# Kernel optimization log

Measured on AMD Instinct MI355X. Metric: run time of the kernel, lower is better.

The kernel has to match this reference:

```python
import jax, jax.numpy as jnp
import numpy as np

HEADS = 4


def setup_inputs() -> dict:
    key = jax.random.key(0)
    kx, kqkv, kbq, ko, kbo = jax.random.split(key, 5)
    B, C, H, W = 4, 256, 64, 64
    x = jax.random.normal(kx, (B, C, H, W), dtype=jnp.float32)
    # torch nn.Linear stores weight as [out_features, in_features]
    w_qkv = jax.random.normal(kqkv, (3 * C, C), dtype=jnp.float32) * (1.0 / np.sqrt(C))
    b_qkv = jax.random.normal(kbq, (3 * C,), dtype=jnp.float32) * 0.02
    w_o = jax.random.normal(ko, (C, C), dtype=jnp.float32) * (1.0 / np.sqrt(C))
    b_o = jax.random.normal(kbo, (C,), dtype=jnp.float32) * 0.02
    return {"x": x, "w_qkv": w_qkv, "b_qkv": b_qkv, "w_o": w_o, "b_o": b_o}


def reference(x, w_qkv, b_qkv, w_o, b_o):
    B, C, H, W = x.shape
    S = H * W
    hd = C // HEADS
    # (B, C, H, W) -> (B, S, C)
    xt = x.reshape(B, C, S).transpose(0, 2, 1)
    qkv = xt @ w_qkv.T + b_qkv                      # (B, S, 3C)
    q, k, v = jnp.split(qkv, 3, axis=-1)
    def to_heads(t):
        return t.reshape(B, S, HEADS, hd).transpose(0, 2, 1, 3)  # (B, h, S, hd)
    q, k, v = to_heads(q), to_heads(k), to_heads(v)
    scores = jnp.einsum('bhqd,bhkd->bhqk', q, k) / jnp.sqrt(jnp.float32(hd))
    attn = jax.nn.softmax(scores, axis=-1)          # dropout inactive (eval)
    out = jnp.einsum('bhqk,bhkd->bhqd', attn, v)    # (B, h, S, hd)
    out = out.transpose(0, 2, 1, 3).reshape(B, S, C)
    y = out @ w_o.T + b_o                            # (B, S, C)
    y = y.reshape(B, H, W, C).transpose(0, 3, 1, 2)  # (B, C, H, W)
    return y
```

## Files before the change

### kernel.cpp

```cpp
#include <hip/hip_runtime.h>
#include <stdint.h>

#define DI __device__ __forceinline__

typedef __attribute__((ext_vector_type(8))) __bf16 bf16x8;
typedef __attribute__((ext_vector_type(8))) unsigned short u16x8;
typedef __attribute__((ext_vector_type(4))) float f32x4;
typedef __attribute__((ext_vector_type(4))) uint32_t u32x4;
typedef unsigned short u16;

constexpr int Bb = 4, Cc = 256, Ss = 4096, HD = 64;
constexpr int ELEMS = Bb * Cc * Ss;

DI float bf2f(u16 h) { union { unsigned u; float f; } x; x.u = ((unsigned)h) << 16; return x.f; }
DI u16 f2bf(float f) {
  union { float f; unsigned u; } x; x.f = f;
  return (u16)((x.u + 0x7FFFu + ((x.u >> 16) & 1u)) >> 16);
}
DI uint32_t pack2bf_trunc(float a, float b) {
  union { float f; uint32_t u; } xa, xb;
  xa.f = a; xb.f = b;
  return __builtin_amdgcn_perm(xb.u, xa.u, 0x07060302u);
}
DI bf16x8 ldfrag(const u16* p) { return __builtin_bit_cast(bf16x8, *(const u16x8*)p); }

__global__ __launch_bounds__(256) void k_transpose(const float* __restrict__ x, u16* __restrict__ xt,
                                                   const float* __restrict__ wq, const float* __restrict__ wo,
                                                   u16* __restrict__ wqb, u16* __restrict__ wob) {
  __shared__ u16 T[64][72];
  const int st = blockIdx.x, ct = blockIdx.y, b = blockIdx.z;
  const int tid = threadIdx.x;
  {
    int flat = blockIdx.x + 64 * blockIdx.y + 256 * blockIdx.z;
    int widx = flat * 256 + tid;
    if (widx < 196608) wqb[widx] = f2bf(wq[widx]);
    else wob[widx - 196608] = f2bf(wo[widx - 196608]);
  }
#pragma unroll
  for (int e = 0; e < 2; e++) {
    int ss = tid + e * 256;
    int r = ss >> 3, seg = ss & 7;
    size_t base = ((size_t)(b * Cc + ct * 64 + r) << 12) + st * 64 + seg * 8;
    u16x8 t;
#pragma unroll
    for (int j = 0; j < 8; j++) t[j] = f2bf(x[base + j]);
    *(u16x8*)&T[r][(seg ^ ((r >> 3) & 7)) * 8] = t;
  }
  __syncthreads();
#pragma unroll
  for (int e = 0; e < 2; e++) {
    int ss = tid + e * 256;
    int sr = ss >> 3, cseg = ss & 7;
    u16x8 o;
#pragma unroll
    for (int j = 0; j < 8; j++) {
      int row = cseg * 8 + j;
      o[j] = T[row][(((sr >> 3) ^ cseg) * 8) + (sr & 7)];
    }
    *(u16x8*)(xt + ((size_t)(b * Ss + st * 64 + sr) << 8) + ct * 64 + cseg * 8) = o;
  }
}

DI void stage_tile(const u16* __restrict__ src, int pitch, int r0, int k0, u16 (*dst)[40], int tid) {
#pragma unroll
  for (int e = 0; e < 2; e++) {
    int c = tid + e * 256;
    int row = c >> 2, seg = c & 3;
    u16x8 t = *(const u16x8*)(src + (size_t)(r0 + row) * pitch + k0 + seg * 8);
    *(u16x8*)&dst[row][seg * 8] = t;
  }
}

__global__ __launch_bounds__(256) void k_qkv(const u16* __restrict__ xt, const u16* __restrict__ w,
                                             const float* __restrict__ bias,
                                             u16* __restrict__ q, u16* __restrict__ kk_, u16* __restrict__ vv_) {
  __shared__ u16 As[128][40], Bs[128][40];
  const int tid = threadIdx.x;
  const int wv = tid >> 6, lane = tid & 63;
  const int wm = wv >> 1, wn = wv & 1;
  const int lr = lane & 15, quad = lane >> 4;
  const int r0 = blockIdx.x * 128;
  const int j0 = blockIdx.y * 128;
  f32x4 acc[4][4] = {};
  for (int k0 = 0; k0 < 256; k0 += 32) {
    __syncthreads();
    stage_tile(xt, 256, r0, k0, As, tid);
    stage_tile(w, 256, j0, k0, Bs, tid);
    __syncthreads();
    bf16x8 a[4], b[4];
#pragma unroll
    for (int mt = 0; mt < 4; mt++) a[mt] = ldfrag(&As[wm * 64 + mt * 16 + lr][quad * 8]);
#pragma unroll
    for (int nt = 0; nt < 4; nt++) b[nt] = ldfrag(&Bs[wn * 64 + nt * 16 + lr][quad * 8]);
#pragma unroll
    for (int mt = 0; mt < 4; mt++)
#pragma unroll
      for (int nt = 0; nt < 4; nt++)
        acc[mt][nt] = __builtin_amdgcn_mfma_f32_16x16x32_bf16(a[mt], b[nt], acc[mt][nt], 0, 0, 0);
  }
#pragma unroll
  for (int nt = 0; nt < 4; nt++) {
    int j = j0 + wn * 64 + nt * 16 + lr;
    float bj = bias[j];
    int part = j >> 8, cc = j & 255, head = cc >> 6, d = cc & 63;
    u16* outp = (part == 0) ? q : (part == 1) ? kk_ : vv_;
    float sc = (part == 0) ? 0.18033688f : 1.0f;
#pragma unroll
    for (int mt = 0; mt < 4; mt++)
#pragma unroll
      for (int rg = 0; rg < 4; rg++) {
        int row = r0 + wm * 64 + mt * 16 + quad * 4 + rg;
        int b_ = row >> 12, s = row & 4095;
        outp[((size_t)((b_ * 4 + head) * Ss + s) << 6) + d] = f2bf((acc[mt][nt][rg] + bj) * sc);
      }
  }
}

__global__ __launch_bounds__(256) void k_vt(const u16* __restrict__ v, u16* __restrict__ vt) {
  __shared__ u16 T[64][72];
  const int chunk = blockIdx.x, bh = blockIdx.y;
  const int tid = threadIdx.x;
#pragma unroll
  for (int e = 0; e < 2; e++) {
    int row = (tid >> 3) + e * 32, seg = tid & 7;
    *(u16x8*)&T[row][(seg ^ ((row >> 3) & 7)) * 8] =
        *(const u16x8*)(v + ((size_t)(bh * Ss + chunk * 64 + row) << 6) + seg * 8);
  }
  __syncthreads();
#pragma unroll
  for (int e = 0; e < 2; e++) {
    int d = (tid >> 3) + e * 32, seg = tid & 7;
    u16x8 o;
#pragma unroll
    for (int j = 0; j < 8; j++) {
      int slot = seg * 8 + j;
      int t = (((slot >> 5) & 1) << 1) | ((slot >> 2) & 1);
      int w6 = t * 16 + (((slot >> 3) & 3) << 2) + (slot & 3);
      o[j] = T[w6][(((d >> 3) ^ ((w6 >> 3) & 7)) * 8) + (d & 7)];
    }
    *(u16x8*)(vt + ((size_t)(bh * 64 + d) << 12) + chunk * 64 + seg * 8) = o;
  }
}

__global__ __launch_bounds__(256, 2) void k_attn(const u16* __restrict__ Q, const u16* __restrict__ K,
                                                 const u16* __restrict__ VT, u16* __restrict__ AO,
                                                 u16* __restrict__ AOP, float* __restrict__ lpart,
                                                 int nsplit) {
  __shared__ u16 Kl[2][64][72];
  __shared__ u16 Vl[2][64][72];
  const int tid = threadIdx.x;
  const int wv = tid >> 6, lane = tid & 63;
  const int lr = lane & 15, quad = lane >> 4;
  const int bh = blockIdx.y;
  const int b_ = bh >> 2, head = bh & 3;
  const int qbase = blockIdx.x * 256 + wv * 64;
  const int sp = blockIdx.z;
  const int nchunk = 64 / nsplit, kcg0 = sp * nchunk;
  const u16* Qh = Q + (size_t)bh * Ss * HD;
  const u16* Kh = K + (size_t)bh * Ss * HD;
  const u16* Vh = VT + (size_t)bh * HD * Ss;

  bf16x8 qb[4][2];
#pragma unroll
  for (int nt = 0; nt < 4; nt++)
#pragma unroll
    for (int ks = 0; ks < 2; ks++)
      qb[nt][ks] = ldfrag(Qh + (size_t)(qbase + nt * 16 + lr) * HD + ks * 32 + quad * 8);

  u16x8 ov;
#pragma unroll
  for (int j = 0; j < 8; j++) ov[j] = 0x3F80;
  const bf16x8 ones = __builtin_bit_cast(bf16x8, ov);

  f32x4 O[4][4] = {};
  f32x4 lacc[4] = {};

  u16x8 pf[4];
  const int srow = tid >> 3, sseg = tid & 7;
  auto load_chunk = [&](int kc) {
#pragma unroll
    for (int e = 0; e < 2; e++) {
      pf[e] = *(const u16x8*)(Kh + ((size_t)((kcg0 + kc) * 64 + srow + e * 32) << 6) + sseg * 8);
      pf[2 + e] = *(const u16x8*)(Vh + ((size_t)(srow + e * 32) << 12) + (kcg0 + kc) * 64 + sseg * 8);
    }
  };
  auto store_chunk = [&](int buf) {
#pragma unroll
    for (int e = 0; e < 2; e++) {
      *(u16x8*)&Kl[buf][srow + e * 32][sseg * 8] = pf[e];
      *(u16x8*)&Vl[buf][srow + e * 32][sseg * 8] = pf[2 + e];
    }
  };

  load_chunk(0);
  store_chunk(0);
  if (nchunk > 1) load_chunk(1);
  __syncthreads();

  for (int kc = 0; kc < nchunk; kc++) {
    const int cur = kc & 1;
    if (kc + 1 < nchunk) {
      store_chunk(cur ^ 1);
      if (kc + 2 < nchunk) load_chunk(kc + 2);
    }

    f32x4 St[4][4] = {};
#pragma unroll
    for (int ks = 0; ks < 2; ks++) {
      bf16x8 ka[4];
#pragma unroll
      for (int kt = 0; kt < 4; kt++) ka[kt] = ldfrag(&Kl[cur][kt * 16 + lr][ks * 32 + quad * 8]);
#pragma unroll
      for (int kt = 0; kt < 4; kt++)
#pragma unroll
        for (int nt = 0; nt < 4; nt++)
          St[kt][nt] = __builtin_amdgcn_mfma_f32_16x16x32_bf16(ka[kt], qb[nt][ks], St[kt][nt], 0, 0, 0);
    }

    uint32_t pk[4][4][2];
#pragma unroll
    for (int kt = 0; kt < 4; kt++)
#pragma unroll
      for (int nt = 0; nt < 4; nt++) {
        float p0 = __builtin_amdgcn_exp2f(St[kt][nt][0]);
        float p1 = __builtin_amdgcn_exp2f(St[kt][nt][1]);
        float p2 = __builtin_amdgcn_exp2f(St[kt][nt][2]);
        float p3 = __builtin_amdgcn_exp2f(St[kt][nt][3]);
        pk[kt][nt][0] = pack2bf_trunc(p0, p1);
        pk[kt][nt][1] = pack2bf_trunc(p2, p3);
      }

#pragma unroll
    for (int ks = 0; ks < 2; ks++) {
      bf16x8 pa[4];
#pragma unroll
      for (int mt = 0; mt < 4; mt++) {
        u32x4 t = {pk[2 * ks][mt][0], pk[2 * ks][mt][1], pk[2 * ks + 1][mt][0], pk[2 * ks + 1][mt][1]};
        pa[mt] = __builtin_bit_cast(bf16x8, t);
      }
#pragma unroll
      for (int dt = 0; dt < 4; dt++) {
        bf16x8 vb = ldfrag(&Vl[cur][dt * 16 + lr][ks * 32 + quad * 8]);
#pragma unroll
        for (int mt = 0; mt < 4; mt++)
          O[mt][dt] = __builtin_amdgcn_mfma_f32_16x16x32_bf16(pa[mt], vb, O[mt][dt], 0, 0, 0);
      }
#pragma unroll
      for (int mt = 0; mt < 4; mt++)
        lacc[mt] = __builtin_amdgcn_mfma_f32_16x16x32_bf16(pa[mt], ones, lacc[mt], 0, 0, 0);
    }

    __syncthreads();
  }

  u16* dst = (nsplit == 1) ? AO : (AOP + (size_t)sp * ELEMS);
  if (nsplit > 1 && lr == 0) {
    float* lp = lpart + (size_t)sp * (16 * Ss) + bh * Ss;
#pragma unroll
    for (int mt = 0; mt < 4; mt++)
#pragma unroll
      for (int rg = 0; rg < 4; rg++) lp[qbase + mt * 16 + quad * 4 + rg] = lacc[mt][rg];
  }
#pragma unroll
  for (int mt = 0; mt < 4; mt++)
#pragma unroll
    for (int rg = 0; rg < 4; rg++) {
      float inv = 1.0f / lacc[mt][rg];
      int s = qbase + mt * 16 + quad * 4 + rg;
#pragma unroll
      for (int dt = 0; dt < 4; dt++)
        dst[((size_t)(b_ * Ss + s) << 8) + head * 64 + dt * 16 + lr] = f2bf(O[mt][dt][rg] * inv);
    }
}

__global__ __launch_bounds__(512) void k_oproj(const u16* __restrict__ wo, const u16* __restrict__ ao,
                                               const u16* __restrict__ AOP, const float* __restrict__ lpart,
                                               const float* __restrict__ bo, float* __restrict__ y, int nsplit) {
  __shared__ u16 As[256][40], Bs[128][40];
  const int tid = threadIdx.x;
  const int wv = tid >> 6, lane = tid & 63;
  const int wm = wv >> 1, wn = wv & 1;
  const int lr = lane & 15, quad = lane >> 4;
  const int n0 = blockIdx.x * 128;
  f32x4 acc[4][4] = {};
  for (int k0 = 0; k0 < 256; k0 += 32) {
    __syncthreads();
#pragma unroll
    for (int e = 0; e < 2; e++) {
      int c = tid + e * 512;
      int row = c >> 2, seg = c & 3;
      *(u16x8*)&As[row][seg * 8] = *(const u16x8*)(wo + row * 256 + k0 + seg * 8);
    }
    {
      int row = tid >> 2, seg = tid & 3;
      int bs = n0 + row, cc = k0 + seg * 8;
      u16x8 t;
      if (nsplit == 1) {
        t = *(const u16x8*)(ao + ((size_t)bs << 8) + cc);
      } else {
        int b = bs >> 12, s = bs & 4095, head = cc >> 6;
        int li = (b * 4 + head) * Ss + s;
        u16x8 a0 = *(const u16x8*)(AOP + ((size_t)bs << 8) + cc);
        u16x8 a1 = *(const u16x8*)(AOP + (size_t)ELEMS + ((size_t)bs << 8) + cc);
        float l0 = lpart[li], l1 = lpart[16 * Ss + li];
        float inv = 1.0f / (l0 + l1);
        float w0 = l0 * inv, w1 = l1 * inv;
#pragma unroll
        for (int i = 0; i < 8; i++) t[i] = f2bf(w0 * bf2f(a0[i]) + w1 * bf2f(a1[i]));
      }
      *(u16x8*)&Bs[row][seg * 8] = t;
    }
    __syncthreads();
    bf16x8 a[4], b[4];
#pragma unroll
    for (int mt = 0; mt < 4; mt++) a[mt] = ldfrag(&As[wm * 64 + mt * 16 + lr][quad * 8]);
#pragma unroll
    for (int nt = 0; nt < 4; nt++) b[nt] = ldfrag(&Bs[wn * 64 + nt * 16 + lr][quad * 8]);
#pragma unroll
    for (int mt = 0; mt < 4; mt++)
#pragma unroll
      for (int nt = 0; nt < 4; nt++)
        acc[mt][nt] = __builtin_amdgcn_mfma_f32_16x16x32_bf16(a[mt], b[nt], acc[mt][nt], 0, 0, 0);
  }
#pragma unroll
  for (int mt = 0; mt < 4; mt++)
#pragma unroll
    for (int rg = 0; rg < 4; rg++) {
      int c = wm * 64 + mt * 16 + quad * 4 + rg;
      float bc = bo[c];
#pragma unroll
      for (int nt = 0; nt < 4; nt++) {
        int col = n0 + wn * 64 + nt * 16 + lr;
        int b_ = col >> 12, s = col & 4095;
        y[((size_t)(b_ * Cc + c) << 12) + s] = acc[mt][nt][rg] + bc;
      }
    }
}

extern "C" void kernel_launch(void* const* d_in, const int* in_sizes, int n_in,
                              void* d_out, int out_size, void* d_ws, size_t ws_size,
                              hipStream_t stream) {
  const float* x = (const float*)d_in[0];
  const float* w_qkv = (const float*)d_in[1];
  const float* b_qkv = (const float*)d_in[2];
  const float* w_o = (const float*)d_in[3];
  const float* b_o = (const float*)d_in[4];
  float* y = (float*)d_out;
  u16* ws = (u16*)d_ws;
  u16* xt = ws;
  u16* q = ws + (size_t)ELEMS;
  u16* k = ws + (size_t)2 * ELEMS;
  u16* vt = ws + (size_t)3 * ELEMS;
  u16* ao = xt;
  u16* wqb = ws + (size_t)4 * ELEMS;
  u16* wob = wqb + 196608;
  const size_t Wu16 = (size_t)4 * ELEMS + 262144;
  u16* aop = ws + Wu16;
  u16* v = aop;
  float* lpart = (float*)(aop + (size_t)2 * ELEMS);
  const size_t need = (Wu16 + (size_t)2 * ELEMS) * 2 + (size_t)2 * 16 * Ss * 4;
  const int nsplit = (ws_size >= need) ? 2 : 1;

  k_transpose<<<dim3(64, 4, 4), 256, 0, stream>>>(x, xt, w_qkv, w_o, wqb, wob);
  k_qkv<<<dim3(128, 6), 256, 0, stream>>>(xt, wqb, b_qkv, q, k, v);
  k_vt<<<dim3(64, 16), 256, 0, stream>>>(v, vt);
  k_attn<<<dim3(16, 16, nsplit), 256, 0, stream>>>(q, k, vt, ao, aop, lpart, nsplit);
  k_oproj<<<128, 512, 0, stream>>>(wob, ao, aop, lpart, b_o, y, nsplit);
}
```

Baseline: 177.6 us.

## Swizzle attention LDS, raise occupancy, add 4-way KV split, split out-proj grid

The attention kernel drops LDS padding in favour of an XOR swizzle on K/V tiles, raises launch bounds to 4 blocks per CU, and wraps MFMA groups in s_setprio. The KV sequence split becomes generic, choosing 4 splits when the workspace allows, and the combine in the output projection loops over all splits. The output projection now uses 256-thread blocks on a 2D grid over output channels, which doubles the block count. A 4-way split doubles partial-output traffic and combine work in exchange for more parallelism in attention, and the higher occupancy target may force register spills.

```diff
diff --git a/kernel.cpp b/kernel.cpp
--- a/kernel.cpp
+++ b/kernel.cpp
@@ -142,12 +142,12 @@
   }
 }
 
-__global__ __launch_bounds__(256, 2) void k_attn(const u16* __restrict__ Q, const u16* __restrict__ K,
+__global__ __launch_bounds__(256, 4) void k_attn(const u16* __restrict__ Q, const u16* __restrict__ K,
                                                  const u16* __restrict__ VT, u16* __restrict__ AO,
                                                  u16* __restrict__ AOP, float* __restrict__ lpart,
                                                  int nsplit) {
-  __shared__ u16 Kl[2][64][72];
-  __shared__ u16 Vl[2][64][72];
+  __shared__ u16 Kl[2][64][64];
+  __shared__ u16 Vl[2][64][64];
   const int tid = threadIdx.x;
   const int wv = tid >> 6, lane = tid & 63;
   const int lr = lane & 15, quad = lane >> 4;
@@ -177,6 +177,7 @@
 
   u16x8 pf[4];
   const int srow = tid >> 3, sseg = tid & 7;
+  const int sg = (sseg ^ (srow & 7)) * 8;
   auto load_chunk = [&](int kc) {
 #pragma unroll
     for (int e = 0; e < 2; e++) {
@@ -187,8 +188,8 @@
   auto store_chunk = [&](int buf) {
 #pragma unroll
     for (int e = 0; e < 2; e++) {
-      *(u16x8*)&Kl[buf][srow + e * 32][sseg * 8] = pf[e];
-      *(u16x8*)&Vl[buf][srow + e * 32][sseg * 8] = pf[2 + e];
+      *(u16x8*)&Kl[buf][srow + e * 32][sg] = pf[e];
+      *(u16x8*)&Vl[buf][srow + e * 32][sg] = pf[2 + e];
     }
   };
 
@@ -209,12 +210,17 @@
     for (int ks = 0; ks < 2; ks++) {
       bf16x8 ka[4];
 #pragma unroll
-      for (int kt = 0; kt < 4; kt++) ka[kt] = ldfrag(&Kl[cur][kt * 16 + lr][ks * 32 + quad * 8]);
+      for (int kt = 0; kt < 4; kt++) {
+        int g = ((ks * 4 + quad) ^ (lr & 7)) * 8;
+        ka[kt] = ldfrag(&Kl[cur][kt * 16 + lr][g]);
+      }
+      __builtin_amdgcn_s_setprio(1);
 #pragma unroll
       for (int kt = 0; kt < 4; kt++)
 #pragma unroll
         for (int nt = 0; nt < 4; nt++)
           St[kt][nt] = __builtin_amdgcn_mfma_f32_16x16x32_bf16(ka[kt], qb[nt][ks], St[kt][nt], 0, 0, 0);
+      __builtin_amdgcn_s_setprio(0);
     }
 
     uint32_t pk[4][4][2];
@@ -240,10 +246,13 @@
       }
 #pragma unroll
       for (int dt = 0; dt < 4; dt++) {
-        bf16x8 vb = ldfrag(&Vl[cur][dt * 16 + lr][ks * 32 + quad * 8]);
+        int g = ((ks * 4 + quad) ^ (lr & 7)) * 8;
+        bf16x8 vb = ldfrag(&Vl[cur][dt * 16 + lr][g]);
+        __builtin_amdgcn_s_setprio(1);
 #pragma unroll
         for (int mt = 0; mt < 4; mt++)
           O[mt][dt] = __builtin_amdgcn_mfma_f32_16x16x32_bf16(pa[mt], vb, O[mt][dt], 0, 0, 0);
+        __builtin_amdgcn_s_setprio(0);
       }
 #pragma unroll
       for (int mt = 0; mt < 4; mt++)
@@ -273,26 +282,24 @@
     }
 }
 
-__global__ __launch_bounds__(512) void k_oproj(const u16* __restrict__ wo, const u16* __restrict__ ao,
+__global__ __launch_bounds__(256) void k_oproj(const u16* __restrict__ wo, const u16* __restrict__ ao,
                                                const u16* __restrict__ AOP, const float* __restrict__ lpart,
                                                const float* __restrict__ bo, float* __restrict__ y, int nsplit) {
-  __shared__ u16 As[256][40], Bs[128][40];
+  __shared__ u16 As[128][40], Bs[128][40];
   const int tid = threadIdx.x;
   const int wv = tid >> 6, lane = tid & 63;
   const int wm = wv >> 1, wn = wv & 1;
   const int lr = lane & 15, quad = lane >> 4;
   const int n0 = blockIdx.x * 128;
+  const int m0 = blockIdx.y * 128;
   f32x4 acc[4][4] = {};
   for (int k0 = 0; k0 < 256; k0 += 32) {
     __syncthreads();
+    stage_tile(wo, 256, m0, k0, As, tid);
 #pragma unroll
     for (int e = 0; e < 2; e++) {
-      int c = tid + e * 512;
+      int c = tid + e * 256;
       int row = c >> 2, seg = c & 3;
-      *(u16x8*)&As[row][seg * 8] = *(const u16x8*)(wo + row * 256 + k0 + seg * 8);
-    }
-    {
-      int row = tid >> 2, seg = tid & 3;
       int bs = n0 + row, cc = k0 + seg * 8;
       u16x8 t;
       if (nsplit == 1) {
@@ -300,13 +307,18 @@
       } else {
         int b = bs >> 12, s = bs & 4095, head = cc >> 6;
         int li = (b * 4 + head) * Ss + s;
-        u16x8 a0 = *(const u16x8*)(AOP + ((size_t)bs << 8) + cc);
-        u16x8 a1 = *(const u16x8*)(AOP + (size_t)ELEMS + ((size_t)bs << 8) + cc);
-        float l0 = lpart[li], l1 = lpart[16 * Ss + li];
-        float inv = 1.0f / (l0 + l1);
-        float w0 = l0 * inv, w1 = l1 * inv;
-#pragma unroll
-        for (int i = 0; i < 8; i++) t[i] = f2bf(w0 * bf2f(a0[i]) + w1 * bf2f(a1[i]));
+        float accv[8] = {0.f, 0.f, 0.f, 0.f, 0.f, 0.f, 0.f, 0.f};
+        float lsum = 0.f;
+        for (int spl = 0; spl < nsplit; spl++) {
+          float l = lpart[(size_t)spl * (16 * Ss) + li];
+          u16x8 a = *(const u16x8*)(AOP + (size_t)spl * ELEMS + ((size_t)bs << 8) + cc);
+          lsum += l;
+#pragma unroll
+          for (int i = 0; i < 8; i++) accv[i] += l * bf2f(a[i]);
+        }
+        float inv = 1.0f / lsum;
+#pragma unroll
+        for (int i = 0; i < 8; i++) t[i] = f2bf(accv[i] * inv);
       }
       *(u16x8*)&Bs[row][seg * 8] = t;
     }
@@ -326,7 +338,7 @@
   for (int mt = 0; mt < 4; mt++)
 #pragma unroll
     for (int rg = 0; rg < 4; rg++) {
-      int c = wm * 64 + mt * 16 + quad * 4 + rg;
+      int c = m0 + wm * 64 + mt * 16 + quad * 4 + rg;
       float bc = bo[c];
 #pragma unroll
       for (int nt = 0; nt < 4; nt++) {
@@ -355,15 +367,15 @@
   u16* wqb = ws + (size_t)4 * ELEMS;
   u16* wob = wqb + 196608;
   const size_t Wu16 = (size_t)4 * ELEMS + 262144;
+  auto need = [&](int n) { return (Wu16 + (size_t)n * ELEMS) * 2 + (size_t)n * 16 * Ss * 4; };
+  const int nsplit = (ws_size >= need(4)) ? 4 : (ws_size >= need(2)) ? 2 : 1;
   u16* aop = ws + Wu16;
   u16* v = aop;
-  float* lpart = (float*)(aop + (size_t)2 * ELEMS);
-  const size_t need = (Wu16 + (size_t)2 * ELEMS) * 2 + (size_t)2 * 16 * Ss * 4;
-  const int nsplit = (ws_size >= need) ? 2 : 1;
+  float* lpart = (float*)(aop + (size_t)nsplit * ELEMS);
 
   k_transpose<<<dim3(64, 4, 4), 256, 0, stream>>>(x, xt, w_qkv, w_o, wqb, wob);
   k_qkv<<<dim3(128, 6), 256, 0, stream>>>(xt, wqb, b_qkv, q, k, v);
   k_vt<<<dim3(64, 16), 256, 0, stream>>>(v, vt);
   k_attn<<<dim3(16, 16, nsplit), 256, 0, stream>>>(q, k, vt, ao, aop, lpart, nsplit);
-  k_oproj<<<128, 512, 0, stream>>>(wob, ao, aop, lpart, b_o, y, nsplit);
-}
+  k_oproj<<<dim3(128, 2), 256, 0, stream>>>(wob, ao, aop, lpart, b_o, y, nsplit);
+}
```

New measurement: 651.3 us. 267% more time.
